# Performance work log

Measured on AMD Instinct MI355X. Metric: run time of the kernel, lower is better.

## Reference

```python
import jax, jax.numpy as jnp
import numpy as np

BS, NUM_SEG, NUM_SEN = 16, 64, 32
D_MODEL, NUM_HEAD = 1024, 8
D_K = D_MODEL // NUM_HEAD
D_FF = 2 * D_MODEL
EPS = 1e-5


def setup_inputs() -> dict:
    key = jax.random.key(0)
    ks = jax.random.split(key, 16)
    s = 1.0 / np.sqrt(D_MODEL)
    return {
        "A": jax.random.normal(ks[0], (BS, NUM_SEG, D_MODEL), jnp.float32),
        "V": jax.random.normal(ks[1], (BS, NUM_SEG, D_MODEL), jnp.float32),
        "S": jax.random.normal(ks[2], (BS, NUM_SEN, D_MODEL), jnp.float32),
        # Linear weights stored (in, out); torch y = x @ W.T + b is x @ W_io + b here.
        "Wq": jax.random.normal(ks[3], (D_MODEL, D_MODEL), jnp.float32) * s,
        "bq": jnp.zeros((D_MODEL,), jnp.float32),
        "Wk": jax.random.normal(ks[4], (D_MODEL, D_MODEL), jnp.float32) * s,
        "bk": jnp.zeros((D_MODEL,), jnp.float32),
        "Wv": jax.random.normal(ks[5], (D_MODEL, D_MODEL), jnp.float32) * s,
        "bv": jnp.zeros((D_MODEL,), jnp.float32),
        "gamma": jnp.ones((D_MODEL,), jnp.float32),
        "beta": jnp.zeros((D_MODEL,), jnp.float32),
        "W1": jax.random.normal(ks[6], (D_MODEL, D_FF), jnp.float32) * s,
        "b1": jnp.zeros((D_FF,), jnp.float32),
        "W2": jax.random.normal(ks[7], (D_FF, D_MODEL), jnp.float32) * (1.0 / np.sqrt(D_FF)),
        "b2": jnp.zeros((D_MODEL,), jnp.float32),
    }


def _layernorm(x, gamma, beta):
    mu = jnp.mean(x, axis=-1, keepdims=True)
    var = jnp.mean(jnp.square(x - mu), axis=-1, keepdims=True)
    return (x - mu) * jax.lax.rsqrt(var + EPS) * gamma + beta


def reference(A, V, S, Wq, bq, Wk, bk, Wv, bv, gamma, beta, W1, b1, W2, b2):
    bs, num_seg, d = A.shape
    num_sen = S.shape[1]
    H, dk = NUM_HEAD, D_K

    av = jnp.stack([A, V], axis=2)                      # bs, num_seg, 2, d
    v = (av @ Wv + bv).reshape(bs, 1, num_seg, 2, H, dk)
    k = (av @ Wk + bk).reshape(bs, 1, num_seg, 2, H, dk)
    Sn = _layernorm(S, gamma, beta)
    q = (Sn @ Wq + bq).reshape(bs, num_sen, 1, 1, H, dk)

    attn = jnp.sum(q * k, axis=-1, keepdims=True) / np.sqrt(dk).astype(np.float32)
    attn = jax.nn.softmax(attn, axis=-3)                # softmax over A/V modality axis (size 2)
    out = jnp.sum(attn * v, axis=-3)                    # bs, num_sen, num_seg, H, dk
    out = out.reshape(bs, num_sen, num_seg, d)

    # PositionwiseFeedForward (dropout p=0): fc2(relu(fc1(x)))
    out = jax.nn.relu(out @ W1 + b1) @ W2 + b2          # bs, num_sen, num_seg, d
    return out
```

## Files before the change

kernel.cpp:

```cpp
#include <hip/hip_runtime.h>
#include <hip/hip_bf16.h>

#define BSZ 16
#define NSEG 64
#define NSEN 32
#define DM 1024
#define NH 8
#define DKH 128
#define DFF 2048

typedef short bf16x8 __attribute__((ext_vector_type(8)));
typedef float f32x4 __attribute__((ext_vector_type(4)));

__device__ __forceinline__ float b2f(short u) {
  union { unsigned int i; float f; } c;
  c.i = ((unsigned int)(unsigned short)u) << 16;
  return c.f;
}
__device__ __forceinline__ short f2b(float f) {
  __hip_bfloat16 h = __float2bfloat16(f);
  return *reinterpret_cast<short*>(&h);
}

#define SCHED0 __builtin_amdgcn_sched_barrier(0)
#define BAR do { SCHED0; __builtin_amdgcn_s_barrier(); SCHED0; } while (0)

__device__ __forceinline__ void transpose_body(const float* __restrict__ W,
                                               short* __restrict__ Wt,
                                               int K, int N, int bx, int by,
                                               float* tile ) {
  int tx = threadIdx.x & 31, ty = threadIdx.x >> 5;
  int n0 = bx * 32, k0 = by * 32;
#pragma unroll
  for (int i = 0; i < 32; i += 8)
    tile[(ty + i) * 33 + tx] = W[(size_t)(k0 + ty + i) * N + n0 + tx];
  __syncthreads();
#pragma unroll
  for (int i = 0; i < 32; i += 8)
    Wt[(size_t)(n0 + ty + i) * K + k0 + tx] = f2b(tile[tx * 33 + ty + i]);
}

__global__ __launch_bounds__(256) void prep_kernel(
    const float* __restrict__ A, const float* __restrict__ V, short* __restrict__ avbf,
    const float* __restrict__ Wk, short* __restrict__ WkT,
    const float* __restrict__ Wv, short* __restrict__ WvT,
    const float* __restrict__ Wq, short* __restrict__ WqT,
    const float* __restrict__ W1, short* __restrict__ W1T,
    const float* __restrict__ W2, short* __restrict__ W2T,
    const float* __restrict__ S, const float* __restrict__ gamma,
    const float* __restrict__ beta, short* __restrict__ Snbf) {
  __shared__ float smem[32 * 33];
  int bid = blockIdx.x;
  int t = threadIdx.x;
  if (bid < 2048) {
    int i = bid * 256 + t;
    size_t o = (size_t)i * 4;
    int r = (int)(o >> 10);
    int d = (int)(o & 1023);
    int m = r & 1;
    int bseg = r >> 1;
    const float* src = (m ? V : A) + (size_t)bseg * 1024 + d;
    float4 v = *(const float4*)src;
    short4 out;
    out.x = f2b(v.x); out.y = f2b(v.y); out.z = f2b(v.z); out.w = f2b(v.w);
    *(short4*)(avbf + o) = out;
  } else if (bid < 3072) {
    int id = bid - 2048;
    transpose_body(Wk, WkT, 1024, 1024, id & 31, id >> 5, smem);
  } else if (bid < 4096) {
    int id = bid - 3072;
    transpose_body(Wv, WvT, 1024, 1024, id & 31, id >> 5, smem);
  } else if (bid < 5120) {
    int id = bid - 4096;
    transpose_body(Wq, WqT, 1024, 1024, id & 31, id >> 5, smem);
  } else if (bid < 7168) {
    int id = bid - 5120;
    transpose_body(W1, W1T, 1024, 2048, id & 63, id >> 6, smem);
  } else if (bid < 9216) {
    int id = bid - 7168;
    transpose_body(W2, W2T, 2048, 1024, id & 31, id >> 5, smem);
  } else {
    int row = bid - 9216;
    int l = t & 63, w = t >> 6;
    const float* x = S + (size_t)row * 1024;
    float4 v = ((const float4*)x)[t];
    float s = v.x + v.y + v.z + v.w;
#pragma unroll
    for (int off = 32; off; off >>= 1) s += __shfl_down(s, off);
    if (l == 0) smem[w] = s;
    __syncthreads();
    if (t == 0) smem[4] = (smem[0] + smem[1] + smem[2] + smem[3]) * (1.0f / 1024.0f);
    __syncthreads();
    float mean = smem[4];
    float4 c = {v.x - mean, v.y - mean, v.z - mean, v.w - mean};
    float s2 = c.x * c.x + c.y * c.y + c.z * c.z + c.w * c.w;
#pragma unroll
    for (int off = 32; off; off >>= 1) s2 += __shfl_down(s2, off);
    __syncthreads();
    if (l == 0) smem[w] = s2;
    __syncthreads();
    if (t == 0) smem[5] = (smem[0] + smem[1] + smem[2] + smem[3]) * (1.0f / 1024.0f);
    __syncthreads();
    float rstd = rsqrtf(smem[5] + 1e-5f);
    int base = t * 4;
    short4 o;
    o.x = f2b(c.x * rstd * gamma[base + 0] + beta[base + 0]);
    o.y = f2b(c.y * rstd * gamma[base + 1] + beta[base + 1]);
    o.z = f2b(c.z * rstd * gamma[base + 2] + beta[base + 2]);
    o.w = f2b(c.w * rstd * gamma[base + 3] + beta[base + 3]);
    *(short4*)(Snbf + (size_t)row * 1024 + base) = o;
  }
}

__global__ __launch_bounds__(256) void gemm_kvq(const short* __restrict__ avbf,
                                                const short* __restrict__ WkvT,
                                                const float* __restrict__ bk,
                                                const float* __restrict__ bv,
                                                short* __restrict__ kbf,
                                                short* __restrict__ vbf,
                                                const short* __restrict__ Snbf,
                                                const short* __restrict__ WqT,
                                                const float* __restrict__ bq,
                                                short* __restrict__ qbf) {
  constexpr int BK = 32;
  __shared__ short As[128 * BK];
  __shared__ short Bs[128 * BK];
  int bid = blockIdx.x;
  const short *Ab, *Bb;
  const float *biasLo, *biasHi;
  short *Clo, *Chi;
  int bm, bn;
  bool split;
  if (bid < 256) {
    int nb = (bid & 7) * 32 + (bid >> 3);
    bn = nb & 15; bm = nb >> 4;
    Ab = avbf; Bb = WkvT; biasLo = bk; biasHi = bv; Clo = kbf; Chi = vbf; split = true;
  } else {
    int id = bid - 256;
    bm = id >> 3; bn = id & 7;
    Ab = Snbf; Bb = WqT; biasLo = bq; biasHi = bq; Clo = qbf; Chi = qbf; split = false;
  }

  const int t = threadIdx.x, w = t >> 6, l = t & 63;
  const int wm = w >> 1, wn = w & 1;
  f32x4 acc[4][4] = {};
  const size_t brow = (size_t)bm * 128, bcol = (size_t)bn * 128;

  for (int kt = 0; kt < 1024; kt += BK) {
#pragma unroll
    for (int i = 0; i < 2; i++) {
      int s = w * 128 + i * 64 + l;
      int row = s >> 2, c = (s & 3) * 8;
      const short* ga = Ab + (brow + row) * (size_t)1024 + kt + c;
      __builtin_amdgcn_global_load_lds(
          (const __attribute__((address_space(1))) unsigned int*)ga,
          (__attribute__((address_space(3))) unsigned int*)(As + (w * 128 + i * 64) * 8),
          16, 0, 0);
      const short* gb = Bb + (bcol + row) * (size_t)1024 + kt + c;
      __builtin_amdgcn_global_load_lds(
          (const __attribute__((address_space(1))) unsigned int*)gb,
          (__attribute__((address_space(3))) unsigned int*)(Bs + (w * 128 + i * 64) * 8),
          16, 0, 0);
    }
    __syncthreads();
    bf16x8 af[4], bfr[4];
#pragma unroll
    for (int mi = 0; mi < 4; mi++)
      af[mi] = *(const bf16x8*)(As + (wm * 64 + mi * 16 + (l & 15)) * BK + (l >> 4) * 8);
#pragma unroll
    for (int ni = 0; ni < 4; ni++)
      bfr[ni] = *(const bf16x8*)(Bs + (wn * 64 + ni * 16 + (l & 15)) * BK + (l >> 4) * 8);
#pragma unroll
    for (int mi = 0; mi < 4; mi++)
#pragma unroll
      for (int ni = 0; ni < 4; ni++)
        acc[mi][ni] = __builtin_amdgcn_mfma_f32_16x16x32_bf16(af[mi], bfr[ni], acc[mi][ni], 0, 0, 0);
    __syncthreads();
  }

  const int lr = (l >> 4) * 4, lc = l & 15;
#pragma unroll
  for (int mi = 0; mi < 4; mi++) {
#pragma unroll
    for (int ni = 0; ni < 4; ni++) {
      size_t gcol = bcol + wn * 64 + ni * 16 + lc;
      int half = split ? (gcol >= 1024) : 0;
      size_t cc = half ? (gcol - 1024) : gcol;
      const float* bp = half ? biasHi : biasLo;
      short* op = half ? Chi : Clo;
      float bvv = bp[cc];
#pragma unroll
      for (int r = 0; r < 4; r++) {
        size_t grow = brow + wm * 64 + mi * 16 + lr + r;
        op[grow * 1024 + cc] = f2b(acc[mi][ni][r] + bvv);
      }
    }
  }
}

template <int RELU, int OUTBF, int BIAS>
__global__ __launch_bounds__(256) void gemm_bf16(const short* __restrict__ Abf, int lda, long long strideA,
                                                 const short* __restrict__ Btbf, int ldb, long long strideB,
                                                 const float* __restrict__ bias,
                                                 void* __restrict__ Cout, int ldc, long long strideC,
                                                 int M, int N, int K) {
  constexpr int BM = 128, BN = 128, BK = 32;
  __shared__ short As[BM * BK];
  __shared__ short Bs[BN * BK];
  const short* Ab = Abf + (size_t)strideA * blockIdx.z;
  const short* Bb = Btbf + (size_t)strideB * blockIdx.z;

  int nwg = gridDim.x * gridDim.y;
  int L = blockIdx.y * gridDim.x + blockIdx.x;
  int bm, bn;
  if ((nwg & 7) == 0) {
    int cpx = nwg >> 3;
    int nb = (L & 7) * cpx + (L >> 3);
    bn = nb % gridDim.x;
    bm = nb / gridDim.x;
  } else {
    bn = blockIdx.x;
    bm = blockIdx.y;
  }

  const int t = threadIdx.x, w = t >> 6, l = t & 63;
  const int wm = w >> 1, wn = w & 1;
  f32x4 acc[4][4] = {};
  const size_t brow = (size_t)bm * BM, bcol = (size_t)bn * BN;

  for (int kt = 0; kt < K; kt += BK) {
#pragma unroll
    for (int i = 0; i < 2; i++) {
      int s = w * 128 + i * 64 + l;
      int row = s >> 2, c = (s & 3) * 8;
      const short* ga = Ab + (brow + row) * (size_t)lda + kt + c;
      __builtin_amdgcn_global_load_lds(
          (const __attribute__((address_space(1))) unsigned int*)ga,
          (__attribute__((address_space(3))) unsigned int*)(As + (w * 128 + i * 64) * 8),
          16, 0, 0);
      const short* gb = Bb + (bcol + row) * (size_t)ldb + kt + c;
      __builtin_amdgcn_global_load_lds(
          (const __attribute__((address_space(1))) unsigned int*)gb,
          (__attribute__((address_space(3))) unsigned int*)(Bs + (w * 128 + i * 64) * 8),
          16, 0, 0);
    }
    __syncthreads();
    bf16x8 af[4], bfr[4];
#pragma unroll
    for (int mi = 0; mi < 4; mi++)
      af[mi] = *(const bf16x8*)(As + (wm * 64 + mi * 16 + (l & 15)) * BK + (l >> 4) * 8);
#pragma unroll
    for (int ni = 0; ni < 4; ni++)
      bfr[ni] = *(const bf16x8*)(Bs + (wn * 64 + ni * 16 + (l & 15)) * BK + (l >> 4) * 8);
#pragma unroll
    for (int mi = 0; mi < 4; mi++)
#pragma unroll
      for (int ni = 0; ni < 4; ni++)
        acc[mi][ni] = __builtin_amdgcn_mfma_f32_16x16x32_bf16(af[mi], bfr[ni], acc[mi][ni], 0, 0, 0);
    __syncthreads();
  }

  const int lr = (l >> 4) * 4, lc = l & 15;
#pragma unroll
  for (int mi = 0; mi < 4; mi++) {
#pragma unroll
    for (int ni = 0; ni < 4; ni++) {
      size_t gcol = bcol + wn * 64 + ni * 16 + lc;
      float bvv = BIAS ? bias[gcol] : 0.f;
#pragma unroll
      for (int r = 0; r < 4; r++) {
        size_t grow = brow + wm * 64 + mi * 16 + lr + r;
        float val = acc[mi][ni][r] + bvv;
        if (RELU) val = fmaxf(val, 0.f);
        size_t cidx = grow * (size_t)ldc + gcol + (size_t)strideC * blockIdx.z;
        if (OUTBF)
          ((short*)Cout)[cidx] = f2b(val);
        else
          ((float*)Cout)[cidx] = val;
      }
    }
  }
}

template <int RELU, int OUTBF, int BIAS>
__global__ __launch_bounds__(512, 2) void gemm256(const short* __restrict__ Abf, int lda,
                                                  const short* __restrict__ Btbf, int ldb,
                                                  const float* __restrict__ bias,
                                                  void* __restrict__ Cout, int ldc, int K) {
  __shared__ __align__(16) short As[2][256 * 64];
  __shared__ __align__(16) short Bs[2][256 * 64];
  const int t = threadIdx.x;
  const int w = t >> 6, l = t & 63;
  const int wr = w >> 2, wc = w & 3;
  const int l15 = l & 15, lhi = l >> 4;

  int nwg = gridDim.x * gridDim.y;
  int L = blockIdx.y * gridDim.x + blockIdx.x;
  int bm, bn;
  if ((nwg & 7) == 0) {
    int cpx = nwg >> 3;
    int nb = (L & 7) * cpx + (L >> 3);
    bn = nb % gridDim.x;
    bm = nb / gridDim.x;
  } else {
    bn = blockIdx.x;
    bm = blockIdx.y;
  }
  const size_t brow = (size_t)bm * 256, bcol = (size_t)bn * 256;
  const int NT = K >> 6;

  auto stage = [&](short* dst, const short* src, int ld, size_t rowoff, int kt) {
#pragma unroll
    for (int i = 0; i < 4; ++i) {
      int seg = i * 512 + t;
      int row = seg >> 3, s = seg & 7;
      const short* g = src + (rowoff + row) * (size_t)ld + kt + ((s ^ (row & 7)) << 3);
      __builtin_amdgcn_global_load_lds(
          (const __attribute__((address_space(1))) unsigned int*)g,
          (__attribute__((address_space(3))) unsigned int*)(dst + seg * 8),
          16, 0, 0);
    }
  };
  auto rdA = [&](const short* base, int m, int kk) -> bf16x8 {
    int r = wr * 128 + m * 16 + l15;
    int d = kk * 4 + lhi;
    return *(const bf16x8*)(base + (r << 6) + ((d ^ (r & 7)) << 3));
  };
  auto rdB = [&](const short* base, int n, int kk) -> bf16x8 {
    int r = wc * 64 + n * 16 + l15;
    int d = kk * 4 + lhi;
    return *(const bf16x8*)(base + (r << 6) + ((d ^ (r & 7)) << 3));
  };

  f32x4 acc[8][4] = {};
  bf16x8 afr[4][2], bfr[4][2];

  stage(Bs[0], Btbf, ldb, bcol, 0);
  stage(As[0], Abf, lda, brow, 0);
  stage(Bs[1], Btbf, ldb, bcol, 64);
  stage(As[1], Abf, lda, brow, 64);
  asm volatile("s_waitcnt vmcnt(8)" ::: "memory");
  BAR;

  for (int T = 0; T < NT; ++T) {
    const short* Ab = As[T & 1];
    const short* Bb = Bs[T & 1];
    short* Aw = (short*)As[T & 1];
    short* Bw = (short*)Bs[T & 1];
    const int ktn = (T + 2) * 64;
    const bool st = (T + 2) < NT;

#pragma unroll
    for (int m = 0; m < 4; ++m) { afr[m][0] = rdA(Ab, m, 0); afr[m][1] = rdA(Ab, m, 1); }
#pragma unroll
    for (int n = 0; n < 2; ++n) { bfr[n][0] = rdB(Bb, n, 0); bfr[n][1] = rdB(Bb, n, 1); }
    BAR;
    __builtin_amdgcn_s_setprio(1);
#pragma unroll
    for (int m = 0; m < 4; ++m)
#pragma unroll
      for (int n = 0; n < 2; ++n) {
        acc[m][n] = __builtin_amdgcn_mfma_f32_16x16x32_bf16(afr[m][0], bfr[n][0], acc[m][n], 0, 0, 0);
        acc[m][n] = __builtin_amdgcn_mfma_f32_16x16x32_bf16(afr[m][1], bfr[n][1], acc[m][n], 0, 0, 0);
      }
    __builtin_amdgcn_s_setprio(0);
    BAR;

#pragma unroll
    for (int n = 2; n < 4; ++n) { bfr[n][0] = rdB(Bb, n, 0); bfr[n][1] = rdB(Bb, n, 1); }
    BAR;
    __builtin_amdgcn_s_setprio(1);
#pragma unroll
    for (int m = 0; m < 4; ++m)
#pragma unroll
      for (int n = 2; n < 4; ++n) {
        acc[m][n] = __builtin_amdgcn_mfma_f32_16x16x32_bf16(afr[m][0], bfr[n][0], acc[m][n], 0, 0, 0);
        acc[m][n] = __builtin_amdgcn_mfma_f32_16x16x32_bf16(afr[m][1], bfr[n][1], acc[m][n], 0, 0, 0);
      }
    __builtin_amdgcn_s_setprio(0);
    BAR;

#pragma unroll
    for (int m = 0; m < 4; ++m) { afr[m][0] = rdA(Ab, m + 4, 0); afr[m][1] = rdA(Ab, m + 4, 1); }
    if (st) stage(Bw, Btbf, ldb, bcol, ktn);
    BAR;
    __builtin_amdgcn_s_setprio(1);
#pragma unroll
    for (int m = 0; m < 4; ++m)
#pragma unroll
      for (int n = 0; n < 2; ++n) {
        acc[m + 4][n] = __builtin_amdgcn_mfma_f32_16x16x32_bf16(afr[m][0], bfr[n][0], acc[m + 4][n], 0, 0, 0);
        acc[m + 4][n] = __builtin_amdgcn_mfma_f32_16x16x32_bf16(afr[m][1], bfr[n][1], acc[m + 4][n], 0, 0, 0);
      }
    __builtin_amdgcn_s_setprio(0);
    BAR;

    if (st) stage(Aw, Abf, lda, brow, ktn);
    __builtin_amdgcn_s_setprio(1);
#pragma unroll
    for (int m = 0; m < 4; ++m)
#pragma unroll
      for (int n = 2; n < 4; ++n) {
        acc[m + 4][n] = __builtin_amdgcn_mfma_f32_16x16x32_bf16(afr[m][0], bfr[n][0], acc[m + 4][n], 0, 0, 0);
        acc[m + 4][n] = __builtin_amdgcn_mfma_f32_16x16x32_bf16(afr[m][1], bfr[n][1], acc[m + 4][n], 0, 0, 0);
      }
    __builtin_amdgcn_s_setprio(0);
    if (st) { asm volatile("s_waitcnt vmcnt(8)" ::: "memory"); }
    else    { asm volatile("s_waitcnt vmcnt(0)" ::: "memory"); }
    BAR;
  }

#pragma unroll
  for (int m = 0; m < 8; ++m) {
#pragma unroll
    for (int n = 0; n < 4; ++n) {
      size_t col = bcol + wc * 64 + n * 16 + l15;
      float bvv = BIAS ? bias[col] : 0.f;
#pragma unroll
      for (int r = 0; r < 4; ++r) {
        size_t row = brow + wr * 128 + m * 16 + lhi * 4 + r;
        float val = acc[m][n][r] + bvv;
        if (RELU) val = fmaxf(val, 0.f);
        if (OUTBF)
          ((short*)Cout)[row * (size_t)ldc + col] = f2b(val);
        else
          ((float*)Cout)[row * (size_t)ldc + col] = val;
      }
    }
  }
}

__global__ __launch_bounds__(256) void attn_p_kernel(const short* __restrict__ qbf,
                                                     const short* __restrict__ kbf,
                                                     float* __restrict__ p) {
  int blk = blockIdx.x;
  int b = blk >> 5;
  __shared__ float qs[1024];
  __shared__ float ss[1024];
  int t = threadIdx.x;
  {
    short4 qv = *(const short4*)(qbf + (size_t)blk * 1024 + t * 4);
    qs[t * 4 + 0] = b2f(qv.x);
    qs[t * 4 + 1] = b2f(qv.y);
    qs[t * 4 + 2] = b2f(qv.z);
    qs[t * 4 + 3] = b2f(qv.w);
  }
  __syncthreads();
  float sc[4];
#pragma unroll
  for (int i = 0; i < 4; i++) {
    int idx = i * 256 + t;
    int seg = idx >> 4, h = (idx >> 1) & 7, m = idx & 1;
    const short* kp = kbf + ((size_t)((b * 64 + seg) * 2 + m)) * 1024 + h * 128;
    float s = 0.f;
#pragma unroll
    for (int j = 0; j < 16; j++) {
      bf16x8 kv = *(const bf16x8*)(kp + j * 8);
#pragma unroll
      for (int e = 0; e < 8; e++) s += qs[h * 128 + j * 8 + e] * b2f(kv[e]);
    }
    sc[i] = s * 0.08838834764831845f;
  }
#pragma unroll
  for (int i = 0; i < 4; i++) ss[i * 256 + t] = sc[i];
  __syncthreads();
  for (int i = t; i < 512; i += 256) {
    float s0 = ss[2 * i], s1 = ss[2 * i + 1];
    float mx = fmaxf(s0, s1);
    float e0 = __expf(s0 - mx), e1 = __expf(s1 - mx);
    float inv = 1.f / (e0 + e1);
    int seg = i >> 3, h = i & 7;
    size_t base = (size_t)blk * 1024 + seg * 16;
    p[base + h] = e0 * inv;
    p[base + 8 + h] = e1 * inv;
  }
}

__global__ __launch_bounds__(512) void mix_kernel(const short* __restrict__ u,
                                                  const float* __restrict__ p,
                                                  const float* __restrict__ b1,
                                                  short* __restrict__ H) {
  int blk = blockIdx.x;
  int b = blk >> 6, seg = blk & 63;
  int t = threadIdx.x;
  __shared__ float ps[512];
  {
    int sen = t >> 4, j = t & 15;
    ps[t] = p[(size_t)(b * 32 + sen) * 1024 + seg * 16 + j];
  }
  int f0 = t * 4;
  float ur[16][4];
#pragma unroll
  for (int mh = 0; mh < 16; ++mh) {
    int m = mh >> 3, h = mh & 7;
    const short* up = u + ((size_t)(blk * 2 + m)) * 16384 + h * 2048 + f0;
    short4 uv = *(const short4*)up;
    ur[mh][0] = b2f(uv.x); ur[mh][1] = b2f(uv.y);
    ur[mh][2] = b2f(uv.z); ur[mh][3] = b2f(uv.w);
  }
  float4 bb = *(const float4*)(b1 + f0);
  __syncthreads();
  for (int sen = 0; sen < 32; ++sen) {
    float a0 = bb.x, a1 = bb.y, a2 = bb.z, a3 = bb.w;
#pragma unroll
    for (int mh = 0; mh < 16; ++mh) {
      float wv = ps[sen * 16 + mh];
      a0 += wv * ur[mh][0];
      a1 += wv * ur[mh][1];
      a2 += wv * ur[mh][2];
      a3 += wv * ur[mh][3];
    }
    short4 o;
    o.x = f2b(fmaxf(a0, 0.f));
    o.y = f2b(fmaxf(a1, 0.f));
    o.z = f2b(fmaxf(a2, 0.f));
    o.w = f2b(fmaxf(a3, 0.f));
    size_t row = (size_t)(b * 32 + sen) * 64 + seg;
    *(short4*)(H + row * 2048 + f0) = o;
  }
}

extern "C" void kernel_launch(void* const* d_in, const int* in_sizes, int n_in,
                              void* d_out, int out_size, void* d_ws, size_t ws_size,
                              hipStream_t stream) {
  const float* A = (const float*)d_in[0];
  const float* V = (const float*)d_in[1];
  const float* S = (const float*)d_in[2];
  const float* Wq = (const float*)d_in[3];
  const float* bq = (const float*)d_in[4];
  const float* Wk = (const float*)d_in[5];
  const float* bk = (const float*)d_in[6];
  const float* Wv = (const float*)d_in[7];
  const float* bv = (const float*)d_in[8];
  const float* gamma = (const float*)d_in[9];
  const float* beta = (const float*)d_in[10];
  const float* W1 = (const float*)d_in[11];
  const float* b1 = (const float*)d_in[12];
  const float* W2 = (const float*)d_in[13];
  const float* b2 = (const float*)d_in[14];

  const size_t MiB = 1048576;
  char* ws = (char*)d_ws;
  short* avbf = (short*)(ws + 0 * MiB);
  short* WkT  = (short*)(ws + 4 * MiB);
  short* WvT  = (short*)(ws + 6 * MiB);
  short* WqT  = (short*)(ws + 8 * MiB);
  short* W1T  = (short*)(ws + 10 * MiB);
  short* W2T  = (short*)(ws + 14 * MiB);
  short* Snbf = (short*)(ws + 18 * MiB);
  short* kbf  = (short*)(ws + 19 * MiB);
  short* vbf  = (short*)(ws + 23 * MiB);
  short* qbf  = (short*)(ws + 27 * MiB);
  float* pbuf = (float*)(ws + 28 * MiB);
  short* ubuf = (short*)(ws + 30 * MiB);
  short* Hbf  = (short*)(ws + 94 * MiB);

  prep_kernel<<<9728, 256, 0, stream>>>(A, V, avbf, Wk, WkT, Wv, WvT, Wq, WqT,
                                        W1, W1T, W2, W2T, S, gamma, beta, Snbf);

  gemm_kvq<<<288, 256, 0, stream>>>(avbf, WkT, bk, bv, kbf, vbf, Snbf, WqT, bq, qbf);

  gemm_bf16<0, 1, 0><<<dim3(16, 16, 8), 256, 0, stream>>>(vbf, 1024, 128, W1T, 1024, 128,
                                                          nullptr, ubuf, 16384, 2048,
                                                          2048, 2048, 128);

  attn_p_kernel<<<512, 256, 0, stream>>>(qbf, kbf, pbuf);

  mix_kernel<<<1024, 512, 0, stream>>>(ubuf, pbuf, b1, Hbf);

  gemm256<0, 0, 1><<<dim3(4, 128), 512, 0, stream>>>(Hbf, 2048, W2T, 2048, b2,
                                                     (float*)d_out, 1024, 2048);
}
```

Baseline: 301.9 us.

## Simplify gemm256 main loop to single-stage prefetch with one barrier per tile

Replaces the two-tile-ahead, four-phase ping-pong main loop (with setprio and several barriers per K-step) with a simpler loop. It issues the next tile's global-to-LDS loads first, then reads all B fragments and streams A fragments through the full 8x4 MFMA block, and ends with a full vmcnt(0) wait and one barrier. Launch bounds drop to one workgroup per CU, which allows more registers but lowers occupancy. The aim is fewer barriers and less scheduling overhead. The cost is a shallower prefetch and less overlap between memory and MFMA.

```diff
diff --git a/kernel.cpp b/kernel.cpp
--- a/kernel.cpp
+++ b/kernel.cpp
@@ -283,7 +283,7 @@
 }
 
 template <int RELU, int OUTBF, int BIAS>
-__global__ __launch_bounds__(512, 2) void gemm256(const short* __restrict__ Abf, int lda,
+__global__ __launch_bounds__(512, 1) void gemm256(const short* __restrict__ Abf, int lda,
                                                   const short* __restrict__ Btbf, int ldb,
                                                   const float* __restrict__ bias,
                                                   void* __restrict__ Cout, int ldc, int K) {
@@ -333,80 +333,40 @@
   };
 
   f32x4 acc[8][4] = {};
-  bf16x8 afr[4][2], bfr[4][2];
 
   stage(Bs[0], Btbf, ldb, bcol, 0);
   stage(As[0], Abf, lda, brow, 0);
-  stage(Bs[1], Btbf, ldb, bcol, 64);
-  stage(As[1], Abf, lda, brow, 64);
-  asm volatile("s_waitcnt vmcnt(8)" ::: "memory");
+  asm volatile("s_waitcnt vmcnt(0)" ::: "memory");
   BAR;
 
   for (int T = 0; T < NT; ++T) {
     const short* Ab = As[T & 1];
     const short* Bb = Bs[T & 1];
-    short* Aw = (short*)As[T & 1];
-    short* Bw = (short*)Bs[T & 1];
-    const int ktn = (T + 2) * 64;
-    const bool st = (T + 2) < NT;
-
-#pragma unroll
-    for (int m = 0; m < 4; ++m) { afr[m][0] = rdA(Ab, m, 0); afr[m][1] = rdA(Ab, m, 1); }
-#pragma unroll
-    for (int n = 0; n < 2; ++n) { bfr[n][0] = rdB(Bb, n, 0); bfr[n][1] = rdB(Bb, n, 1); }
-    BAR;
-    __builtin_amdgcn_s_setprio(1);
-#pragma unroll
-    for (int m = 0; m < 4; ++m)
-#pragma unroll
-      for (int n = 0; n < 2; ++n) {
-        acc[m][n] = __builtin_amdgcn_mfma_f32_16x16x32_bf16(afr[m][0], bfr[n][0], acc[m][n], 0, 0, 0);
-        acc[m][n] = __builtin_amdgcn_mfma_f32_16x16x32_bf16(afr[m][1], bfr[n][1], acc[m][n], 0, 0, 0);
+    short* Anx = (short*)As[(T + 1) & 1];
+    short* Bnx = (short*)Bs[(T + 1) & 1];
+    const bool st = (T + 1) < NT;
+
+    if (st) {
+      stage(Bnx, Btbf, ldb, bcol, (T + 1) * 64);
+      stage(Anx, Abf, lda, brow, (T + 1) * 64);
+    }
+    SCHED0;
+
+    bf16x8 bf[4][2];
+#pragma unroll
+    for (int n = 0; n < 4; ++n) { bf[n][0] = rdB(Bb, n, 0); bf[n][1] = rdB(Bb, n, 1); }
+#pragma unroll
+    for (int m = 0; m < 8; ++m) {
+      bf16x8 a0 = rdA(Ab, m, 0);
+      bf16x8 a1 = rdA(Ab, m, 1);
+#pragma unroll
+      for (int n = 0; n < 4; ++n) {
+        acc[m][n] = __builtin_amdgcn_mfma_f32_16x16x32_bf16(a0, bf[n][0], acc[m][n], 0, 0, 0);
+        acc[m][n] = __builtin_amdgcn_mfma_f32_16x16x32_bf16(a1, bf[n][1], acc[m][n], 0, 0, 0);
       }
-    __builtin_amdgcn_s_setprio(0);
-    BAR;
-
-#pragma unroll
-    for (int n = 2; n < 4; ++n) { bfr[n][0] = rdB(Bb, n, 0); bfr[n][1] = rdB(Bb, n, 1); }
-    BAR;
-    __builtin_amdgcn_s_setprio(1);
-#pragma unroll
-    for (int m = 0; m < 4; ++m)
-#pragma unroll
-      for (int n = 2; n < 4; ++n) {
-        acc[m][n] = __builtin_amdgcn_mfma_f32_16x16x32_bf16(afr[m][0], bfr[n][0], acc[m][n], 0, 0, 0);
-        acc[m][n] = __builtin_amdgcn_mfma_f32_16x16x32_bf16(afr[m][1], bfr[n][1], acc[m][n], 0, 0, 0);
-      }
-    __builtin_amdgcn_s_setprio(0);
-    BAR;
-
-#pragma unroll
-    for (int m = 0; m < 4; ++m) { afr[m][0] = rdA(Ab, m + 4, 0); afr[m][1] = rdA(Ab, m + 4, 1); }
-    if (st) stage(Bw, Btbf, ldb, bcol, ktn);
-    BAR;
-    __builtin_amdgcn_s_setprio(1);
-#pragma unroll
-    for (int m = 0; m < 4; ++m)
-#pragma unroll
-      for (int n = 0; n < 2; ++n) {
-        acc[m + 4][n] = __builtin_amdgcn_mfma_f32_16x16x32_bf16(afr[m][0], bfr[n][0], acc[m + 4][n], 0, 0, 0);
-        acc[m + 4][n] = __builtin_amdgcn_mfma_f32_16x16x32_bf16(afr[m][1], bfr[n][1], acc[m + 4][n], 0, 0, 0);
-      }
-    __builtin_amdgcn_s_setprio(0);
-    BAR;
-
-    if (st) stage(Aw, Abf, lda, brow, ktn);
-    __builtin_amdgcn_s_setprio(1);
-#pragma unroll
-    for (int m = 0; m < 4; ++m)
-#pragma unroll
-      for (int n = 2; n < 4; ++n) {
-        acc[m + 4][n] = __builtin_amdgcn_mfma_f32_16x16x32_bf16(afr[m][0], bfr[n][0], acc[m + 4][n], 0, 0, 0);
-        acc[m + 4][n] = __builtin_amdgcn_mfma_f32_16x16x32_bf16(afr[m][1], bfr[n][1], acc[m + 4][n], 0, 0, 0);
-      }
-    __builtin_amdgcn_s_setprio(0);
-    if (st) { asm volatile("s_waitcnt vmcnt(8)" ::: "memory"); }
-    else    { asm volatile("s_waitcnt vmcnt(0)" ::: "memory"); }
+    }
+
+    asm volatile("s_waitcnt vmcnt(0)" ::: "memory");
     BAR;
   }
 
```

Result: no change. 305.3 us (+1.1%).

## Software-pipeline LDS fragment reads across GEMM K-tiles with split register sets

Applied to the files above, without the earlier changes.

Restructures the main GEMM loop so each LDS fragment read overlaps with MFMAs on registers loaded earlier. Separate A0/A1 and B0/B1 register sets are used, and the next tile's first fragments are prefetched before the last MFMA quadrant. This drops about two barriers per iteration and changes the vmcnt waits to match the new ordering of global-to-LDS stages. It costs more VGPRs, which may lower occupancy, and it adds subtle hazards in the ordering between LDS writes and reads.

```diff
diff --git a/kernel.cpp b/kernel.cpp
--- a/kernel.cpp
+++ b/kernel.cpp
@@ -333,7 +333,7 @@
   };
 
   f32x4 acc[8][4] = {};
-  bf16x8 afr[4][2], bfr[4][2];
+  bf16x8 A0[4][2], A1[4][2], B0[2][2], B1[2][2];
 
   stage(Bs[0], Btbf, ldb, bcol, 0);
   stage(As[0], Abf, lda, brow, 0);
@@ -341,72 +341,78 @@
   stage(As[1], Abf, lda, brow, 64);
   asm volatile("s_waitcnt vmcnt(8)" ::: "memory");
   BAR;
+#pragma unroll
+  for (int m = 0; m < 4; ++m) { A0[m][0] = rdA(As[0], m, 0); A0[m][1] = rdA(As[0], m, 1); }
+#pragma unroll
+  for (int n = 0; n < 2; ++n) { B0[n][0] = rdB(Bs[0], n, 0); B0[n][1] = rdB(Bs[0], n, 1); }
 
   for (int T = 0; T < NT; ++T) {
     const short* Ab = As[T & 1];
     const short* Bb = Bs[T & 1];
     short* Aw = (short*)As[T & 1];
     short* Bw = (short*)Bs[T & 1];
+    const short* An = As[(T + 1) & 1];
+    const short* Bn = Bs[(T + 1) & 1];
     const int ktn = (T + 2) * 64;
     const bool st = (T + 2) < NT;
-
-#pragma unroll
-    for (int m = 0; m < 4; ++m) { afr[m][0] = rdA(Ab, m, 0); afr[m][1] = rdA(Ab, m, 1); }
-#pragma unroll
-    for (int n = 0; n < 2; ++n) { bfr[n][0] = rdB(Bb, n, 0); bfr[n][1] = rdB(Bb, n, 1); }
-    BAR;
+    const bool rd = (T + 1) < NT;
+
+#pragma unroll
+    for (int j = 0; j < 2; ++j) { B1[j][0] = rdB(Bb, j + 2, 0); B1[j][1] = rdB(Bb, j + 2, 1); }
     __builtin_amdgcn_s_setprio(1);
 #pragma unroll
     for (int m = 0; m < 4; ++m)
 #pragma unroll
       for (int n = 0; n < 2; ++n) {
-        acc[m][n] = __builtin_amdgcn_mfma_f32_16x16x32_bf16(afr[m][0], bfr[n][0], acc[m][n], 0, 0, 0);
-        acc[m][n] = __builtin_amdgcn_mfma_f32_16x16x32_bf16(afr[m][1], bfr[n][1], acc[m][n], 0, 0, 0);
+        acc[m][n] = __builtin_amdgcn_mfma_f32_16x16x32_bf16(A0[m][0], B0[n][0], acc[m][n], 0, 0, 0);
+        acc[m][n] = __builtin_amdgcn_mfma_f32_16x16x32_bf16(A0[m][1], B0[n][1], acc[m][n], 0, 0, 0);
       }
     __builtin_amdgcn_s_setprio(0);
     BAR;
 
 #pragma unroll
-    for (int n = 2; n < 4; ++n) { bfr[n][0] = rdB(Bb, n, 0); bfr[n][1] = rdB(Bb, n, 1); }
-    BAR;
+    for (int m = 0; m < 4; ++m) { A1[m][0] = rdA(Ab, m + 4, 0); A1[m][1] = rdA(Ab, m + 4, 1); }
     __builtin_amdgcn_s_setprio(1);
 #pragma unroll
     for (int m = 0; m < 4; ++m)
 #pragma unroll
-      for (int n = 2; n < 4; ++n) {
-        acc[m][n] = __builtin_amdgcn_mfma_f32_16x16x32_bf16(afr[m][0], bfr[n][0], acc[m][n], 0, 0, 0);
-        acc[m][n] = __builtin_amdgcn_mfma_f32_16x16x32_bf16(afr[m][1], bfr[n][1], acc[m][n], 0, 0, 0);
+      for (int j = 0; j < 2; ++j) {
+        acc[m][j + 2] = __builtin_amdgcn_mfma_f32_16x16x32_bf16(A0[m][0], B1[j][0], acc[m][j + 2], 0, 0, 0);
+        acc[m][j + 2] = __builtin_amdgcn_mfma_f32_16x16x32_bf16(A0[m][1], B1[j][1], acc[m][j + 2], 0, 0, 0);
       }
     __builtin_amdgcn_s_setprio(0);
     BAR;
 
-#pragma unroll
-    for (int m = 0; m < 4; ++m) { afr[m][0] = rdA(Ab, m + 4, 0); afr[m][1] = rdA(Ab, m + 4, 1); }
     if (st) stage(Bw, Btbf, ldb, bcol, ktn);
+    __builtin_amdgcn_s_setprio(1);
+#pragma unroll
+    for (int m = 0; m < 4; ++m)
+#pragma unroll
+      for (int n = 0; n < 2; ++n) {
+        acc[m + 4][n] = __builtin_amdgcn_mfma_f32_16x16x32_bf16(A1[m][0], B0[n][0], acc[m + 4][n], 0, 0, 0);
+        acc[m + 4][n] = __builtin_amdgcn_mfma_f32_16x16x32_bf16(A1[m][1], B0[n][1], acc[m + 4][n], 0, 0, 0);
+      }
+    __builtin_amdgcn_s_setprio(0);
+    if (st)      { asm volatile("s_waitcnt vmcnt(4)" ::: "memory"); }
+    else if (rd) { asm volatile("s_waitcnt vmcnt(0)" ::: "memory"); }
     BAR;
+
+    if (st) stage(Aw, Abf, lda, brow, ktn);
+    if (rd) {
+#pragma unroll
+      for (int m = 0; m < 4; ++m) { A0[m][0] = rdA(An, m, 0); A0[m][1] = rdA(An, m, 1); }
+#pragma unroll
+      for (int n = 0; n < 2; ++n) { B0[n][0] = rdB(Bn, n, 0); B0[n][1] = rdB(Bn, n, 1); }
+    }
     __builtin_amdgcn_s_setprio(1);
 #pragma unroll
     for (int m = 0; m < 4; ++m)
 #pragma unroll
-      for (int n = 0; n < 2; ++n) {
-        acc[m + 4][n] = __builtin_amdgcn_mfma_f32_16x16x32_bf16(afr[m][0], bfr[n][0], acc[m + 4][n], 0, 0, 0);
-        acc[m + 4][n] = __builtin_amdgcn_mfma_f32_16x16x32_bf16(afr[m][1], bfr[n][1], acc[m + 4][n], 0, 0, 0);
+      for (int j = 0; j < 2; ++j) {
+        acc[m + 4][j + 2] = __builtin_amdgcn_mfma_f32_16x16x32_bf16(A1[m][0], B1[j][0], acc[m + 4][j + 2], 0, 0, 0);
+        acc[m + 4][j + 2] = __builtin_amdgcn_mfma_f32_16x16x32_bf16(A1[m][1], B1[j][1], acc[m + 4][j + 2], 0, 0, 0);
       }
     __builtin_amdgcn_s_setprio(0);
-    BAR;
-
-    if (st) stage(Aw, Abf, lda, brow, ktn);
-    __builtin_amdgcn_s_setprio(1);
-#pragma unroll
-    for (int m = 0; m < 4; ++m)
-#pragma unroll
-      for (int n = 2; n < 4; ++n) {
-        acc[m + 4][n] = __builtin_amdgcn_mfma_f32_16x16x32_bf16(afr[m][0], bfr[n][0], acc[m + 4][n], 0, 0, 0);
-        acc[m + 4][n] = __builtin_amdgcn_mfma_f32_16x16x32_bf16(afr[m][1], bfr[n][1], acc[m + 4][n], 0, 0, 0);
-      }
-    __builtin_amdgcn_s_setprio(0);
-    if (st) { asm volatile("s_waitcnt vmcnt(8)" ::: "memory"); }
-    else    { asm volatile("s_waitcnt vmcnt(0)" ::: "memory"); }
     BAR;
   }
 
```

Result: slower. 316.3 us (+4.8%).
